# Performance work log

Measured on AMD Instinct MI355X. Metric: run time of the kernel, lower is better.

## Reference

```python
import jax, jax.numpy as jnp
import numpy as np

B, T, C = 2, 2048, 1024
N_HEAD = 16
HEAD_DIM = C // N_HEAD


def setup_inputs() -> dict:
    key = jax.random.key(0)
    k1, k2, k3, k4, k5 = jax.random.split(key, 5)
    s = 1.0 / np.sqrt(C)
    return {
        "x": jax.random.normal(k1, (B, T, C), dtype=jnp.float32),
        "w_attn": jax.random.normal(k2, (C, 3 * C), dtype=jnp.float32) * s,
        "b_attn": jax.random.normal(k3, (3 * C,), dtype=jnp.float32) * 0.02,
        "w_proj": jax.random.normal(k4, (C, C), dtype=jnp.float32) * s,
        "b_proj": jax.random.normal(k5, (C,), dtype=jnp.float32) * 0.02,
    }


def reference(x, w_attn, b_attn, w_proj, b_proj):
    Bx, Tx, Cx = x.shape
    qkv = x @ w_attn + b_attn  # [B, T, 3C]
    q, k, v = jnp.split(qkv, 3, axis=2)
    # [B, H, T, D]
    q = q.reshape(Bx, Tx, N_HEAD, HEAD_DIM).transpose(0, 2, 1, 3)
    k = k.reshape(Bx, Tx, N_HEAD, HEAD_DIM).transpose(0, 2, 1, 3)
    v = v.reshape(Bx, Tx, N_HEAD, HEAD_DIM).transpose(0, 2, 1, 3)
    scale = 1.0 / jnp.sqrt(jnp.asarray(HEAD_DIM, dtype=x.dtype))
    att = jnp.einsum("bhqd,bhkd->bhqk", q, k) * scale  # [B,H,T,T]
    causal = jnp.tril(jnp.ones((Tx, Tx), dtype=bool))
    att = jnp.where(causal[None, None, :, :], att, -jnp.inf)
    att = jax.nn.softmax(att, axis=-1)
    y = jnp.einsum("bhqk,bhkd->bhqd", att, v)  # [B,H,T,D]
    y = y.transpose(0, 2, 1, 3).reshape(Bx, Tx, Cx)
    return y @ w_proj + b_proj
```

## Files before the change

### kernel.cpp

```cpp
#include <hip/hip_runtime.h>
#include <hip/hip_bf16.h>
#include <stdint.h>

#define TT 2048
#define CC 1024
#define NH 16
#define HD 64
#define BT 4096

typedef float f32x4 __attribute__((ext_vector_type(4)));
typedef __bf16 bf16x8 __attribute__((ext_vector_type(8)));
typedef __bf16 bf16x4 __attribute__((ext_vector_type(4)));

#define MFMA(a, b, c) __builtin_amdgcn_mfma_f32_16x16x32_bf16((a), (b), (c), 0, 0, 0)

__device__ __forceinline__ void gload16(const void* g, void* l) {
    __builtin_amdgcn_global_load_lds(
        (const __attribute__((address_space(1))) void*)g,
        (__attribute__((address_space(3))) void*)l,
        16, 0, 0);
}

__global__ __launch_bounds__(256) void conv_f32_bf16(
    const float* __restrict__ in, __bf16* __restrict__ out, int n4) {
    int i = blockIdx.x * blockDim.x + threadIdx.x;
    int stride = gridDim.x * blockDim.x;
    for (; i < n4; i += stride) {
        float4 v = reinterpret_cast<const float4*>(in)[i];
        bf16x4 o;
        o.x = (__bf16)v.x; o.y = (__bf16)v.y; o.z = (__bf16)v.z; o.w = (__bf16)v.w;
        reinterpret_cast<bf16x4*>(out)[i] = o;
    }
}

__global__ __launch_bounds__(256) void transpose_f32_bf16(
    const float* __restrict__ in, __bf16* __restrict__ out, int R, int C) {
    __shared__ float tile[32][33];
    int c0 = blockIdx.x * 32, r0 = blockIdx.y * 32;
    int tx = threadIdx.x, ty = threadIdx.y;
#pragma unroll
    for (int j = 0; j < 32; j += 8)
        tile[ty + j][tx] = in[(size_t)(r0 + ty + j) * C + c0 + tx];
    __syncthreads();
#pragma unroll
    for (int j = 0; j < 32; j += 8)
        out[(size_t)(c0 + ty + j) * R + r0 + tx] = (__bf16)tile[tx][ty + j];
}

template <int MODE>
__global__ __launch_bounds__(256) void gemm128(
    const __bf16* __restrict__ A, const __bf16* __restrict__ Bt,
    const float* __restrict__ bias,
    __bf16* __restrict__ oq, __bf16* __restrict__ ok, __bf16* __restrict__ ov,
    float* __restrict__ of, int M, int N, int K) {
    __shared__ __align__(16) __bf16 As[128 * 64];
    __shared__ __align__(16) __bf16 Bs[128 * 64];
    const int tid = threadIdx.x;
    const int w = tid >> 6, lane = tid & 63;
    const int l15 = lane & 15, lg = lane >> 4;
    const int m0 = blockIdx.y * 128, n0 = blockIdx.x * 128;
    const int wr = w >> 1, wc = w & 1;

    const f32x4 zero4 = {0.f, 0.f, 0.f, 0.f};
    f32x4 acc[4][4];
#pragma unroll
    for (int m = 0; m < 4; ++m)
#pragma unroll
        for (int n = 0; n < 4; ++n) acc[m][n] = zero4;

    const char* Ab = (const char*)A;
    const char* Bb = (const char*)Bt;
    const size_t rowbytes = (size_t)K * 2;

    for (int kt = 0; kt < K; kt += 64) {
#pragma unroll
        for (int j = 0; j < 4; ++j) {
            int base = (w * 4 + j) * 1024;
            int d0 = base + lane * 16;
            int row = d0 >> 7;
            int colb = d0 & 127;
            int scolb = colb ^ ((row & 7) << 4);
            gload16(Ab + (size_t)(m0 + row) * rowbytes + (size_t)kt * 2 + scolb,
                    (char*)As + base);
            gload16(Bb + (size_t)(n0 + row) * rowbytes + (size_t)kt * 2 + scolb,
                    (char*)Bs + base);
        }
        __syncthreads();
#pragma unroll
        for (int kk = 0; kk < 2; ++kk) {
            bf16x8 af[4], bfr[4];
#pragma unroll
            for (int m = 0; m < 4; ++m) {
                int row = wr * 64 + m * 16 + l15;
                int colb = kk * 64 + lg * 16;
                af[m] = *(const bf16x8*)((const char*)As + row * 128 +
                                         (colb ^ ((row & 7) << 4)));
            }
#pragma unroll
            for (int n = 0; n < 4; ++n) {
                int row = wc * 64 + n * 16 + l15;
                int colb = kk * 64 + lg * 16;
                bfr[n] = *(const bf16x8*)((const char*)Bs + row * 128 +
                                          (colb ^ ((row & 7) << 4)));
            }
#pragma unroll
            for (int m = 0; m < 4; ++m)
#pragma unroll
                for (int n = 0; n < 4; ++n)
                    acc[m][n] = MFMA(af[m], bfr[n], acc[m][n]);
        }
        __syncthreads();
    }

#pragma unroll
    for (int n = 0; n < 4; ++n) {
        int col = n0 + wc * 64 + n * 16 + l15;
        float bs = bias[col];
        if constexpr (MODE == 0) {
            int sec = col >> 10;
            int cc = col & 1023;
            int h = cc >> 6, d = cc & 63;
            if (sec == 2) {
#pragma unroll
                for (int m = 0; m < 4; ++m) {
                    int rowb = m0 + wr * 64 + m * 16 + lg * 4;
                    int bb = rowb >> 11, t = rowb & 2047;
                    bf16x4 pk;
#pragma unroll
                    for (int r = 0; r < 4; ++r) pk[r] = (__bf16)(acc[m][n][r] + bs);
                    *(bf16x4*)&ov[((size_t)(bb * NH + h) * HD + d) * TT + t] = pk;
                }
            } else {
                __bf16* dst = (sec == 0) ? oq : ok;
                float mult = (sec == 0) ? 0.125f * 1.44269504088896340736f : 1.0f;
#pragma unroll
                for (int m = 0; m < 4; ++m) {
                    int rowb = m0 + wr * 64 + m * 16 + lg * 4;
#pragma unroll
                    for (int r = 0; r < 4; ++r) {
                        int row = rowb + r;
                        int bb = row >> 11, t = row & 2047;
                        float val = (acc[m][n][r] + bs) * mult;
                        dst[((size_t)(bb * NH + h) * TT + t) * HD + d] = (__bf16)val;
                    }
                }
            }
        } else {
#pragma unroll
            for (int m = 0; m < 4; ++m) {
                int rowb = m0 + wr * 64 + m * 16 + lg * 4;
#pragma unroll
                for (int r = 0; r < 4; ++r) {
                    int row = rowb + r;
                    of[(size_t)row * N + col] = acc[m][n][r] + bs;
                }
            }
        }
    }
}

__global__ __launch_bounds__(256) void attn_kernel(
    const __bf16* __restrict__ q, const __bf16* __restrict__ k,
    const __bf16* __restrict__ vt, __bf16* __restrict__ y) {
    __shared__ __align__(16) __bf16 Kb[2][64 * 64];
    __shared__ __align__(16) __bf16 Vb[2][64 * 64];
    __shared__ __align__(16) __bf16 Pl[4][16 * 68];

    const int n = blockIdx.x;
    const int qt = 31 - (n >> 5);
    const int bh = ((n & 7) << 2) | ((n >> 3) & 3);
    const int tid = threadIdx.x, w = tid >> 6, lane = tid & 63;
    const int l15 = lane & 15, lg = lane >> 4;
    const char* kh = (const char*)(k + (size_t)bh * TT * HD);
    const char* vh = (const char*)(vt + (size_t)bh * HD * TT);
    const __bf16* qh = q + (size_t)bh * TT * HD;
    const int qbw = qt * 64 + w * 16;

    const f32x4 zero4 = {0.f, 0.f, 0.f, 0.f};
    float mrun = -1e30f, lrun = 0.f;
    f32x4 oacc[4];
    bf16x8 qf[2];
#pragma unroll
    for (int f = 0; f < 4; ++f) oacc[f] = zero4;
#pragma unroll
    for (int kk = 0; kk < 2; ++kk)
        qf[kk] = *(const bf16x8*)&qh[(size_t)(qbw + l15) * HD + kk * 32 + lg * 8];

    auto stage = [&](int kvb, int buf) {
#pragma unroll
        for (int j = 0; j < 2; ++j) {
            int d0 = ((w * 2 + j) * 64 + lane) * 16;
            int row = d0 >> 7, colb = d0 & 127;
            int scolb = colb ^ ((row & 7) << 4);
            gload16(kh + (size_t)(kvb + row) * 128 + scolb, (char*)Kb[buf] + d0);
            gload16(vh + (size_t)row * (TT * 2) + (size_t)kvb * 2 + scolb,
                    (char*)Vb[buf] + d0);
        }
    };

    stage(0, 0);
    __syncthreads();

    for (int g = 0; g <= qt; ++g) {
        const int cur = g & 1;
        if (g < qt) stage((g + 1) * 64, cur ^ 1);
        const int kb = g * 64;

        f32x4 s[4];
#pragma unroll
        for (int kf = 0; kf < 4; ++kf) s[kf] = zero4;
        __builtin_amdgcn_s_setprio(1);
#pragma unroll
        for (int kf = 0; kf < 4; ++kf) {
            int krow = kf * 16 + l15;
            const char* kr = (const char*)Kb[cur] + krow * 128;
            bf16x8 k0 = *(const bf16x8*)(kr + ((lg * 16) ^ ((krow & 7) << 4)));
            bf16x8 k1 = *(const bf16x8*)(kr + ((64 + lg * 16) ^ ((krow & 7) << 4)));
            s[kf] = MFMA(k0, qf[0], s[kf]);
            s[kf] = MFMA(k1, qf[1], s[kf]);
        }
        __builtin_amdgcn_s_setprio(0);
        if (g == qt) {
            const int qq = qbw + l15;
#pragma unroll
            for (int kf = 0; kf < 4; ++kf)
#pragma unroll
                for (int r = 0; r < 4; ++r) {
                    int kk_ = kb + kf * 16 + lg * 4 + r;
                    if (kk_ > qq) s[kf][r] = -1e30f;
                }
        }
        f32x4 m01, m23;
#pragma unroll
        for (int r = 0; r < 4; ++r) {
            m01[r] = fmaxf(s[0][r], s[1][r]);
            m23[r] = fmaxf(s[2][r], s[3][r]);
        }
        float m_ = fmaxf(fmaxf(fmaxf(m01[0], m01[1]), fmaxf(m01[2], m01[3])),
                         fmaxf(fmaxf(m23[0], m23[1]), fmaxf(m23[2], m23[3])));
        m_ = fmaxf(m_, __shfl_xor(m_, 16));
        m_ = fmaxf(m_, __shfl_xor(m_, 32));
        if (!__all(m_ <= mrun)) {
            float mn = fmaxf(mrun, m_);
            float fac = exp2f(mrun - mn);
            mrun = mn;
            lrun *= fac;
#pragma unroll
            for (int f = 0; f < 4; ++f)
#pragma unroll
                for (int r = 0; r < 4; ++r) oacc[f][r] *= fac;
        }
        float ss = 0.f;
#pragma unroll
        for (int kf = 0; kf < 4; ++kf)
#pragma unroll
            for (int r = 0; r < 4; ++r) {
                float p = exp2f(s[kf][r] - mrun);
                s[kf][r] = p;
                ss += p;
            }
        lrun += ss;
#pragma unroll
        for (int kf = 0; kf < 4; ++kf) {
            bf16x4 pk;
#pragma unroll
            for (int r = 0; r < 4; ++r) pk[r] = (__bf16)s[kf][r];
            *(bf16x4*)&Pl[w][l15 * 68 + kf * 16 + lg * 4] = pk;
        }
        __builtin_amdgcn_s_setprio(1);
#pragma unroll
        for (int kq = 0; kq < 2; ++kq) {
            bf16x8 pfrag = *(const bf16x8*)&Pl[w][l15 * 68 + kq * 32 + lg * 8];
#pragma unroll
            for (int f = 0; f < 4; ++f) {
                int vrow = f * 16 + l15;
                bf16x8 vf = *(const bf16x8*)((const char*)Vb[cur] + vrow * 128 +
                                ((kq * 64 + lg * 16) ^ ((vrow & 7) << 4)));
                oacc[f] = MFMA(vf, pfrag, oacc[f]);
            }
        }
        __builtin_amdgcn_s_setprio(0);
        __syncthreads();
    }

    lrun += __shfl_xor(lrun, 16);
    lrun += __shfl_xor(lrun, 32);
    const int b = bh >> 4, h = bh & 15;
    float inv = 1.0f / lrun;
#pragma unroll
    for (int f = 0; f < 4; ++f) {
        bf16x4 pk;
#pragma unroll
        for (int r = 0; r < 4; ++r) pk[r] = (__bf16)(oacc[f][r] * inv);
        *(bf16x4*)&y[(size_t)(b * TT + qbw + l15) * CC + h * 64 + f * 16 +
                     lg * 4] = pk;
    }
}

extern "C" void kernel_launch(void* const* d_in, const int* in_sizes, int n_in,
                              void* d_out, int out_size, void* d_ws, size_t ws_size,
                              hipStream_t stream) {
    const float* x      = (const float*)d_in[0];
    const float* w_attn = (const float*)d_in[1];
    const float* b_attn = (const float*)d_in[2];
    const float* w_proj = (const float*)d_in[3];
    const float* b_proj = (const float*)d_in[4];
    float* out = (float*)d_out;

    char* ws = (char*)d_ws;
    size_t off = 0;
    auto alloc = [&](size_t bytes) {
        char* p = ws + off;
        off += (bytes + 255) & ~(size_t)255;
        return p;
    };
    __bf16* xb   = (__bf16*)alloc((size_t)BT * CC * 2);
    __bf16* watb = (__bf16*)alloc((size_t)3 * CC * CC * 2);
    __bf16* wptb = (__bf16*)alloc((size_t)CC * CC * 2);
    __bf16* qb   = (__bf16*)alloc((size_t)BT * CC * 2);
    __bf16* kbuf = (__bf16*)alloc((size_t)BT * CC * 2);
    __bf16* vtb  = (__bf16*)alloc((size_t)BT * CC * 2);
    __bf16* yb   = (__bf16*)alloc((size_t)BT * CC * 2);

    conv_f32_bf16<<<1024, 256, 0, stream>>>(x, xb, BT * CC / 4);
    transpose_f32_bf16<<<dim3(3 * CC / 32, CC / 32), dim3(32, 8), 0, stream>>>(
        w_attn, watb, CC, 3 * CC);
    transpose_f32_bf16<<<dim3(CC / 32, CC / 32), dim3(32, 8), 0, stream>>>(
        w_proj, wptb, CC, CC);

    gemm128<0><<<dim3(3 * CC / 128, BT / 128), 256, 0, stream>>>(
        xb, watb, b_attn, qb, kbuf, vtb, nullptr, BT, 3 * CC, CC);

    attn_kernel<<<1024, 256, 0, stream>>>(qb, kbuf, vtb, yb);

    gemm128<1><<<dim3(CC / 128, BT / 128), 256, 0, stream>>>(
        yb, wptb, b_proj, nullptr, nullptr, nullptr, out, BT, CC, CC);
}
```

Baseline: 117.2 us.

## Feed softmax probabilities to PV MFMA from registers and merge weight transposes

The attention kernel no longer writes the softmax probabilities to LDS and reads them back as MFMA operands. The accumulator layout of the QK^T output is reused directly as the B operand of 16x16x16 bf16 MFMAs, which removes the per-tile LDS round trip and the P scratch buffer. In exchange the PV step issues twice as many smaller MFMAs, with 8-byte V loads from LDS. Separately, the two weight transpose launches are merged into one kernel launch.

```diff
diff --git a/kernel.cpp b/kernel.cpp
--- a/kernel.cpp
+++ b/kernel.cpp
@@ -11,8 +11,10 @@
 typedef float f32x4 __attribute__((ext_vector_type(4)));
 typedef __bf16 bf16x8 __attribute__((ext_vector_type(8)));
 typedef __bf16 bf16x4 __attribute__((ext_vector_type(4)));
+typedef short sh4 __attribute__((ext_vector_type(4)));
 
 #define MFMA(a, b, c) __builtin_amdgcn_mfma_f32_16x16x32_bf16((a), (b), (c), 0, 0, 0)
+#define MFMA16(a, b, c) __builtin_amdgcn_mfma_f32_16x16x16bf16_1k((a), (b), (c), 0, 0, 0)
 
 __device__ __forceinline__ void gload16(const void* g, void* l) {
     __builtin_amdgcn_global_load_lds(
@@ -33,18 +35,25 @@
     }
 }
 
-__global__ __launch_bounds__(256) void transpose_f32_bf16(
-    const float* __restrict__ in, __bf16* __restrict__ out, int R, int C) {
+__global__ __launch_bounds__(256) void transpose2_f32_bf16(
+    const float* __restrict__ wa, __bf16* __restrict__ oa,
+    const float* __restrict__ wp, __bf16* __restrict__ op) {
     __shared__ float tile[32][33];
-    int c0 = blockIdx.x * 32, r0 = blockIdx.y * 32;
-    int tx = threadIdx.x, ty = threadIdx.y;
+    int bx = blockIdx.x;
+    const float* in;
+    __bf16* out;
+    int C;
+    if (bx < 96) { in = wa; out = oa; C = 3072; }
+    else         { in = wp; out = op; C = 1024; bx -= 96; }
+    int c0 = bx * 32, r0 = blockIdx.y * 32;
+    int tx = threadIdx.x & 31, ty = (threadIdx.x >> 5) & 7;
 #pragma unroll
     for (int j = 0; j < 32; j += 8)
         tile[ty + j][tx] = in[(size_t)(r0 + ty + j) * C + c0 + tx];
     __syncthreads();
 #pragma unroll
     for (int j = 0; j < 32; j += 8)
-        out[(size_t)(c0 + ty + j) * R + r0 + tx] = (__bf16)tile[tx][ty + j];
+        out[(size_t)(c0 + ty + j) * 1024 + r0 + tx] = (__bf16)tile[tx][ty + j];
 }
 
 template <int MODE>
@@ -164,7 +173,6 @@
     const __bf16* __restrict__ vt, __bf16* __restrict__ y) {
     __shared__ __align__(16) __bf16 Kb[2][64 * 64];
     __shared__ __align__(16) __bf16 Vb[2][64 * 64];
-    __shared__ __align__(16) __bf16 Pl[4][16 * 68];
 
     const int n = blockIdx.x;
     const int qt = 31 - (n >> 5);
@@ -251,32 +259,28 @@
                 for (int r = 0; r < 4; ++r) oacc[f][r] *= fac;
         }
         float ss = 0.f;
-#pragma unroll
-        for (int kf = 0; kf < 4; ++kf)
+        sh4 pb[4];
+#pragma unroll
+        for (int kf = 0; kf < 4; ++kf) {
+            bf16x4 pk;
 #pragma unroll
             for (int r = 0; r < 4; ++r) {
                 float p = exp2f(s[kf][r] - mrun);
-                s[kf][r] = p;
+                pk[r] = (__bf16)p;
                 ss += p;
             }
+            pb[kf] = __builtin_bit_cast(sh4, pk);
+        }
         lrun += ss;
+        __builtin_amdgcn_s_setprio(1);
 #pragma unroll
         for (int kf = 0; kf < 4; ++kf) {
-            bf16x4 pk;
-#pragma unroll
-            for (int r = 0; r < 4; ++r) pk[r] = (__bf16)s[kf][r];
-            *(bf16x4*)&Pl[w][l15 * 68 + kf * 16 + lg * 4] = pk;
-        }
-        __builtin_amdgcn_s_setprio(1);
-#pragma unroll
-        for (int kq = 0; kq < 2; ++kq) {
-            bf16x8 pfrag = *(const bf16x8*)&Pl[w][l15 * 68 + kq * 32 + lg * 8];
 #pragma unroll
             for (int f = 0; f < 4; ++f) {
                 int vrow = f * 16 + l15;
-                bf16x8 vf = *(const bf16x8*)((const char*)Vb[cur] + vrow * 128 +
-                                ((kq * 64 + lg * 16) ^ ((vrow & 7) << 4)));
-                oacc[f] = MFMA(vf, pfrag, oacc[f]);
+                bf16x4 va = *(const bf16x4*)((const char*)Vb[cur] + vrow * 128 +
+                                ((kf * 32 + lg * 8) ^ ((vrow & 7) << 4)));
+                oacc[f] = MFMA16(__builtin_bit_cast(sh4, va), pb[kf], oacc[f]);
             }
         }
         __builtin_amdgcn_s_setprio(0);
@@ -323,10 +327,8 @@
     __bf16* yb   = (__bf16*)alloc((size_t)BT * CC * 2);
 
     conv_f32_bf16<<<1024, 256, 0, stream>>>(x, xb, BT * CC / 4);
-    transpose_f32_bf16<<<dim3(3 * CC / 32, CC / 32), dim3(32, 8), 0, stream>>>(
-        w_attn, watb, CC, 3 * CC);
-    transpose_f32_bf16<<<dim3(CC / 32, CC / 32), dim3(32, 8), 0, stream>>>(
-        w_proj, wptb, CC, CC);
+    transpose2_f32_bf16<<<dim3(128, 32), 256, 0, stream>>>(
+        w_attn, watb, w_proj, wptb);
 
     gemm128<0><<<dim3(3 * CC / 128, BT / 128), 256, 0, stream>>>(
         xb, watb, b_attn, qb, kbuf, vtb, nullptr, BT, 3 * CC, CC);
```

After: 118.2 us. No clear change (+0.8%).
